# Performance work log

Hardware: AMD Instinct MI355X
Metric: run time of the kernel (lower is better)

## Reference

```python
import jax, jax.numpy as jnp
import numpy as np


def setup_inputs() -> dict:
    key = jax.random.key(0)
    ks = jax.random.split(key, 10)
    B, C, T, H, W = 8, 128, 8, 32, 32
    Cq = C // 8
    return {
        "x": jax.random.normal(ks[0], (B, C, T, H, W), dtype=jnp.float32),
        "Wq": jax.random.normal(ks[1], (Cq, C), dtype=jnp.float32) * (1.0 / np.sqrt(C)),
        "bq": jax.random.normal(ks[2], (Cq,), dtype=jnp.float32) * 0.02,
        "Wk": jax.random.normal(ks[3], (Cq, C), dtype=jnp.float32) * (1.0 / np.sqrt(C)),
        "bk": jax.random.normal(ks[4], (Cq,), dtype=jnp.float32) * 0.02,
        "Wv": jax.random.normal(ks[5], (C, C), dtype=jnp.float32) * (1.0 / np.sqrt(C)),
        "bv": jax.random.normal(ks[6], (C,), dtype=jnp.float32) * 0.02,
        "gamma_pam": jax.random.normal(ks[7], (1,), dtype=jnp.float32),
        "gamma_cam": jax.random.normal(ks[8], (1,), dtype=jnp.float32),
        "gamma_tim": jax.random.normal(ks[9], (1,), dtype=jnp.float32),
    }


def reference(x, Wq, bq, Wk, bk, Wv, bv, gamma_pam, gamma_cam, gamma_tim):
    B, C, T, H, W = x.shape
    HW = H * W

    # ---- PAM: position attention over HW, feature dim = (C//8)*T ----
    # 1x1x1 Conv3d == per-position channel matmul
    q = jnp.einsum('bcthw,oc->bothw', x, Wq) + bq[None, :, None, None, None]
    k = jnp.einsum('bcthw,oc->bothw', x, Wk) + bk[None, :, None, None, None]
    v = jnp.einsum('bcthw,oc->bothw', x, Wv) + bv[None, :, None, None, None]
    qf = q.reshape(B, -1, HW)   # [B, (C//8)*T, HW]
    kf = k.reshape(B, -1, HW)
    vf = v.reshape(B, -1, HW)   # [B, C*T, HW]
    energy = jnp.einsum('bcn,bcm->bnm', qf, kf)          # [B, HW, HW]
    attn = jax.nn.softmax(energy, axis=-1)
    # out = bmm(v, attn^T)
    pam = jnp.einsum('bcm,bnm->bcn', vf, attn).reshape(B, C, T, H, W)
    pam = gamma_pam * pam + x

    # ---- CAM: channel attention (C x C) with negated-energy softmax ----
    xc = x.reshape(B, C, -1)                              # [B, C, T*HW]
    e = jnp.einsum('bcn,bdn->bcd', xc, xc)                # [B, C, C]
    e = jnp.max(e, axis=-1, keepdims=True) - e
    a = jax.nn.softmax(e, axis=-1)
    cam = jnp.einsum('bcd,bdn->bcn', a, xc).reshape(B, C, T, H, W)
    cam = gamma_cam * cam + x

    # ---- TIM: temporal attention (T x T) with negated-energy softmax ----
    xt = jnp.transpose(x, (0, 2, 1, 3, 4)).reshape(B, T, -1)  # [B, T, C*HW]
    e = jnp.einsum('btn,bsn->bts', xt, xt)                # [B, T, T]
    e = jnp.max(e, axis=-1, keepdims=True) - e
    a = jax.nn.softmax(e, axis=-1)
    tim = jnp.einsum('bts,bsn->btn', a, xt).reshape(B, T, C, H, W)
    tim = jnp.transpose(tim, (0, 2, 1, 3, 4))
    tim = gamma_tim * tim + x

    return pam + cam + tim
```

## Files before the change

### kernel.cpp

```cpp
#include <hip/hip_runtime.h>
#include <cstdint>

typedef unsigned short u16;
typedef __attribute__((ext_vector_type(8))) short bf16x8;
typedef __attribute__((ext_vector_type(8))) unsigned short u16x8;
typedef __attribute__((ext_vector_type(4))) float f32x4;

constexpr int B_  = 8;
constexpr int C_  = 128;
constexpr int T_  = 8;
constexpr int HW_ = 1024;
constexpr int P_  = T_ * HW_;
constexpr int F_  = 128;
constexpr int CT_ = C_ * T_;

static __device__ __forceinline__ u16 f2bf(float f) {
    union { float f; unsigned u; } v; v.f = f;
    unsigned r = v.u + 0x7fffu + ((v.u >> 16) & 1u);
    return (u16)(r >> 16);
}
static __device__ __forceinline__ float bf2f(u16 h) {
    union { unsigned u; float f; } v; v.u = ((unsigned)h) << 16;
    return v.f;
}

#define GLOAD16(src, dst)                                                     \
    __builtin_amdgcn_global_load_lds(                                         \
        (const __attribute__((address_space(1))) void*)(src),                 \
        (__attribute__((address_space(3))) void*)(dst), 16, 0, 0)

__global__ __launch_bounds__(256)
void k_tim_gram(const float* __restrict__ x, float* __restrict__ e_t,
                const float* __restrict__ Wq, const float* __restrict__ Wk,
                const float* __restrict__ Wv, u16* __restrict__ Wall)
{
    const int b = blockIdx.y, cc = blockIdx.x;
    const int tid = threadIdx.x;

    if (cc == 0 && b == 0) {
        for (int i = tid; i < 20480; i += 256) {
            int oc = i >> 7, c2 = i & 127;
            float wv;
            if (oc < 16)      wv = Wq[oc * 128 + c2];
            else if (oc < 32) wv = Wk[(oc - 16) * 128 + c2];
            else              wv = Wv[(oc - 32) * 128 + c2];
            Wall[i] = f2bf(wv);
        }
    }

    const int hw = tid * 4;
    float4 xv[2][8];
    #pragma unroll
    for (int ci = 0; ci < 2; ci++) {
        const float* xb = x + ((size_t)(b * C_ + cc * 2 + ci)) * P_;
        #pragma unroll
        for (int t = 0; t < 8; t++)
            xv[ci][t] = *(const float4*)&xb[t * HW_ + hw];
    }

    float acc[36];
    #pragma unroll
    for (int p = 0; p < 36; p++) acc[p] = 0.f;
    #pragma unroll
    for (int ci = 0; ci < 2; ci++) {
        int p = 0;
        #pragma unroll
        for (int t = 0; t < 8; t++)
            #pragma unroll
            for (int s = t; s < 8; s++) {
                float4 a = xv[ci][t], c4 = xv[ci][s];
                acc[p++] += a.x * c4.x + a.y * c4.y + a.z * c4.z + a.w * c4.w;
            }
    }

    const int lane = tid & 63, w = tid >> 6;
    #pragma unroll
    for (int p = 0; p < 36; p++)
        #pragma unroll
        for (int off = 32; off; off >>= 1)
            acc[p] += __shfl_xor(acc[p], off);

    __shared__ float sm[4][36];
    if (lane == 0)
        #pragma unroll
        for (int p = 0; p < 36; p++) sm[w][p] = acc[p];
    __syncthreads();
    if (tid < 36) {
        float v = sm[0][tid] + sm[1][tid] + sm[2][tid] + sm[3][tid];
        int t = 0, rem = tid;
        while (rem >= 8 - t) { rem -= 8 - t; t++; }
        int s = t + rem;
        atomicAdd(&e_t[b * 64 + t * 8 + s], v);
        if (s != t) atomicAdd(&e_t[b * 64 + s * 8 + t], v);
    }
}

__global__ __launch_bounds__(256)
void k_prep(const float* __restrict__ x, u16* __restrict__ xT,
            u16* __restrict__ xhi, u16* __restrict__ xlo,
            const u16* __restrict__ Wall,
            const float* __restrict__ bq, const float* __restrict__ bk,
            const float* __restrict__ bv,
            u16* __restrict__ qt, u16* __restrict__ kt, u16* __restrict__ v16)
{
    __shared__ char sy[32768];
    const int b  = blockIdx.y;
    const int p0 = blockIdx.x * 128;
    const int tid = threadIdx.x, lane = tid & 63, w = tid >> 6;

    #pragma unroll
    for (int r = 0; r < 16; r++) {
        int lin = r * 256 + tid;
        int c = lin >> 5, j4 = (lin & 31) << 2;
        size_t gi = ((size_t)(b * C_ + c)) * P_ + p0 + j4;
        float4 xv = *(const float4*)&x[gi];
        float a4[4] = {xv.x, xv.y, xv.z, xv.w};
        ushort4 h, l;
        h.x = f2bf(a4[0]); h.y = f2bf(a4[1]);
        h.z = f2bf(a4[2]); h.w = f2bf(a4[3]);
        l.x = f2bf(a4[0] - bf2f(h.x)); l.y = f2bf(a4[1] - bf2f(h.y));
        l.z = f2bf(a4[2] - bf2f(h.z)); l.w = f2bf(a4[3] - bf2f(h.w));
        *(ushort4*)&xhi[gi] = h;
        *(ushort4*)&xlo[gi] = l;
        #pragma unroll
        for (int u = 0; u < 4; u++) {
            int pi = j4 + u;
            int byte = pi * 256 + ((c * 2) ^ (((pi >> 2) & 15) << 4));
            *(u16*)(sy + byte) = (u == 0) ? h.x : (u == 1) ? h.y
                               : (u == 2) ? h.z : h.w;
        }
    }
    __syncthreads();

    #pragma unroll
    for (int r = 0; r < 8; r++) {
        int lin = r * 256 + tid;
        int pi = lin >> 4, ci8 = (lin & 15) << 3;
        bf16x8 v = *(const bf16x8*)(sy + pi * 256 +
                                    ((ci8 * 2) ^ (((pi >> 2) & 15) << 4)));
        *(bf16x8*)&xT[((size_t)(b * P_ + p0 + pi)) * C_ + ci8] = v;
    }

    bf16x8 bg[4][2];
    #pragma unroll
    for (int ks = 0; ks < 4; ks++)
        #pragma unroll
        for (int ni = 0; ni < 2; ni++) {
            int p  = w * 32 + ni * 16 + (lane & 15);
            int cb = (ks * 32 + (lane >> 4) * 8) * 2;
            bg[ks][ni] = *(const bf16x8*)(sy + p * 256 +
                              (cb ^ (((p >> 2) & 15) << 4)));
        }
    __syncthreads();

    f32x4 acc[10][2];
    #pragma unroll
    for (int mi = 0; mi < 10; mi++) {
        acc[mi][0] = (f32x4){0.f, 0.f, 0.f, 0.f};
        acc[mi][1] = (f32x4){0.f, 0.f, 0.f, 0.f};
    }

    #pragma unroll
    for (int mi = 0; mi < 10; mi++) {
        #pragma unroll
        for (int ks = 0; ks < 4; ks++) {
            bf16x8 af = *(const bf16x8*)(Wall + (mi * 16 + (lane & 15)) * 128
                                          + ks * 32 + (lane >> 4) * 8);
            acc[mi][0] = __builtin_amdgcn_mfma_f32_16x16x32_bf16(
                af, bg[ks][0], acc[mi][0], 0, 0, 0);
            acc[mi][1] = __builtin_amdgcn_mfma_f32_16x16x32_bf16(
                af, bg[ks][1], acc[mi][1], 0, 0, 0);
        }
    }

    const int t      = p0 >> 10;
    const int hw0    = p0 & 1023;
    const int hwbase = hw0 + w * 32;

    #pragma unroll
    for (int mi = 2; mi < 10; mi++)
        #pragma unroll
        for (int ni = 0; ni < 2; ni++)
            #pragma unroll
            for (int r = 0; r < 4; r++) {
                int oc = mi * 16 + (lane >> 4) * 4 + r;
                int hw = hwbase + ni * 16 + (lane & 15);
                v16[((size_t)(b * C_ + oc - 32)) * P_ + t * HW_ + hw] =
                    f2bf(acc[mi][ni][r] + bv[oc - 32]);
            }

    u16* qk = (u16*)sy;
    #pragma unroll
    for (int mi = 0; mi < 2; mi++)
        #pragma unroll
        for (int ni = 0; ni < 2; ni++) {
            int hwl = w * 32 + ni * 16 + (lane & 15);
            int cq0 = (lane >> 4) * 4;
            ushort4 pk;
            float b0 = (mi == 0) ? bq[cq0 + 0] : bk[cq0 + 0];
            float b1 = (mi == 0) ? bq[cq0 + 1] : bk[cq0 + 1];
            float b2 = (mi == 0) ? bq[cq0 + 2] : bk[cq0 + 2];
            float b3 = (mi == 0) ? bq[cq0 + 3] : bk[cq0 + 3];
            pk.x = f2bf(acc[mi][ni][0] + b0);
            pk.y = f2bf(acc[mi][ni][1] + b1);
            pk.z = f2bf(acc[mi][ni][2] + b2);
            pk.w = f2bf(acc[mi][ni][3] + b3);
            *(ushort4*)&qk[(mi * 128 + hwl) * 24 + cq0] = pk;
        }
    __syncthreads();
    {
        int mi = tid >> 7, hwl = tid & 127;
        u16x8 lo = *(const u16x8*)&qk[(mi * 128 + hwl) * 24 + 0];
        u16x8 hi = *(const u16x8*)&qk[(mi * 128 + hwl) * 24 + 8];
        u16* dst = (mi == 0) ? qt : kt;
        size_t off = ((size_t)b * HW_ + hw0 + hwl) * F_ + t * 16;
        *(u16x8*)&dst[off]     = lo;
        *(u16x8*)&dst[off + 8] = hi;
    }
}

__global__ __launch_bounds__(256)
void k_attn(const u16* __restrict__ qt, const u16* __restrict__ kt,
            u16* __restrict__ A16)
{
    __shared__ u16 ost[16][1032];
    __shared__ float red[4][16];
    const int b  = blockIdx.y;
    const int n0 = blockIdx.x * 16;
    const int tid = threadIdx.x, lane = tid & 63, w = tid >> 6;
    const u16* qb = qt + (size_t)b * HW_ * F_;
    const u16* kb = kt + (size_t)b * HW_ * F_;

    bf16x8 af[4];
    #pragma unroll
    for (int ks = 0; ks < 4; ks++)
        af[ks] = *(const bf16x8*)(qb + (size_t)(n0 + (lane & 15)) * F_
                                  + ks * 32 + (lane >> 4) * 8);

    f32x4 acc[16];
    #pragma unroll
    for (int j = 0; j < 16; j++) acc[j] = (f32x4){0.f, 0.f, 0.f, 0.f};

    #pragma unroll
    for (int j = 0; j < 16; j++) {
        const int m0 = w * 256 + j * 16;
        #pragma unroll
        for (int ks = 0; ks < 4; ks++) {
            bf16x8 bg = *(const bf16x8*)(kb + (size_t)(m0 + (lane & 15)) * F_
                                         + ks * 32 + (lane >> 4) * 8);
            acc[j] = __builtin_amdgcn_mfma_f32_16x16x32_bf16(
                af[ks], bg, acc[j], 0, 0, 0);
        }
    }

    float rmax[4];
    #pragma unroll
    for (int r = 0; r < 4; r++) {
        float m = acc[0][r];
        #pragma unroll
        for (int j = 1; j < 16; j++) m = fmaxf(m, acc[j][r]);
        #pragma unroll
        for (int off = 1; off < 16; off <<= 1) m = fmaxf(m, __shfl_xor(m, off));
        rmax[r] = m;
    }
    if ((lane & 15) == 0)
        #pragma unroll
        for (int r = 0; r < 4; r++) red[w][(lane >> 4) * 4 + r] = rmax[r];
    __syncthreads();
    #pragma unroll
    for (int r = 0; r < 4; r++) {
        int row = (lane >> 4) * 4 + r;
        rmax[r] = fmaxf(fmaxf(red[0][row], red[1][row]),
                        fmaxf(red[2][row], red[3][row]));
    }
    __syncthreads();

    float rsum[4];
    #pragma unroll
    for (int r = 0; r < 4; r++) {
        float s = 0.f;
        #pragma unroll
        for (int j = 0; j < 16; j++) {
            acc[j][r] = __expf(acc[j][r] - rmax[r]);
            s += acc[j][r];
        }
        #pragma unroll
        for (int off = 1; off < 16; off <<= 1) s += __shfl_xor(s, off);
        rsum[r] = s;
    }
    if ((lane & 15) == 0)
        #pragma unroll
        for (int r = 0; r < 4; r++) red[w][(lane >> 4) * 4 + r] = rsum[r];
    __syncthreads();

    #pragma unroll
    for (int r = 0; r < 4; r++) {
        int row = (lane >> 4) * 4 + r;
        float inv = 1.0f / (red[0][row] + red[1][row] +
                            red[2][row] + red[3][row]);
        #pragma unroll
        for (int j = 0; j < 16; j++)
            ost[row][w * 256 + j * 16 + (lane & 15)] = f2bf(acc[j][r] * inv);
    }
    __syncthreads();

    u16* ob = A16 + ((size_t)b * HW_ + n0) * HW_;
    #pragma unroll
    for (int it = 0; it < 8; it++) {
        int lin = it * 256 + tid;
        int row = lin >> 7, g = lin & 127;
        *(u16x8*)&ob[(size_t)row * HW_ + g * 8] = *(const u16x8*)&ost[row][g * 8];
    }
}

__global__ __launch_bounds__(256)
void k_pv(const u16* __restrict__ v16, const u16* __restrict__ A16,
          const float* __restrict__ gamma_pam, u16* __restrict__ pam16)
{
    __shared__ char As[2][16384];
    __shared__ char Bs[2][16384];
    const int b   = blockIdx.z;
    const int ct0 = blockIdx.y * 128, n0 = blockIdx.x * 128;
    const int tid = threadIdx.x, lane = tid & 63, w = tid >> 6;
    const u16* vb = v16 + (size_t)b * CT_ * HW_;
    const u16* ab = A16 + (size_t)b * HW_ * HW_;

    const int s_row = (lane >> 3);
    const int s_col = ((lane & 7) ^ ((lane >> 3) & 7)) * 8;

    const int wr = w >> 1, wc = w & 1;
    f32x4 acc[4][4];
    #pragma unroll
    for (int mi = 0; mi < 4; mi++)
        #pragma unroll
        for (int ni = 0; ni < 4; ni++) acc[mi][ni] = (f32x4){0.f, 0.f, 0.f, 0.f};

    #pragma unroll
    for (int i = 0; i < 4; i++) {
        int c = w * 4 + i;
        int row = c * 8 + s_row;
        GLOAD16(vb + (size_t)(ct0 + row) * HW_ + s_col, As[0] + c * 1024);
        GLOAD16(ab + (size_t)(n0  + row) * HW_ + s_col, Bs[0] + c * 1024);
    }
    __syncthreads();

    int cur = 0;
    for (int it = 0; it < 16; ++it) {
        if (it < 15) {
            int mc = (it + 1) * 64;
            #pragma unroll
            for (int i = 0; i < 4; i++) {
                int c = w * 4 + i;
                int row = c * 8 + s_row;
                GLOAD16(vb + (size_t)(ct0 + row) * HW_ + mc + s_col,
                        As[cur ^ 1] + c * 1024);
                GLOAD16(ab + (size_t)(n0  + row) * HW_ + mc + s_col,
                        Bs[cur ^ 1] + c * 1024);
            }
        }
        const char* Ac = As[cur];
        const char* Bc = Bs[cur];
        #pragma unroll
        for (int ks = 0; ks < 2; ks++) {
            bf16x8 af[4], bg[4];
            #pragma unroll
            for (int mi = 0; mi < 4; mi++) {
                int row  = wr * 64 + mi * 16 + (lane & 15);
                int slot = (ks * 4 + (lane >> 4)) ^ (row & 7);
                af[mi] = *(const bf16x8*)(Ac + row * 128 + slot * 16);
                int rb  = wc * 64 + mi * 16 + (lane & 15);
                int sb  = (ks * 4 + (lane >> 4)) ^ (rb & 7);
                bg[mi] = *(const bf16x8*)(Bc + rb * 128 + sb * 16);
            }
            #pragma unroll
            for (int mi = 0; mi < 4; mi++)
                #pragma unroll
                for (int ni = 0; ni < 4; ni++)
                    acc[mi][ni] = __builtin_amdgcn_mfma_f32_16x16x32_bf16(
                        af[mi], bg[ni], acc[mi][ni], 0, 0, 0);
        }
        __syncthreads();
        cur ^= 1;
    }

    const float gp = gamma_pam[0];
    u16* ot = (u16*)As;
    #pragma unroll
    for (int mi = 0; mi < 4; mi++)
        #pragma unroll
        for (int ni = 0; ni < 4; ni++)
            #pragma unroll
            for (int r = 0; r < 4; r++)
                ot[(wr * 64 + mi * 16 + (lane >> 4) * 4 + r) * 128 +
                   wc * 64 + ni * 16 + (lane & 15)] = f2bf(gp * acc[mi][ni][r]);
    __syncthreads();

    u16* ob = pam16 + (size_t)b * CT_ * HW_;
    #pragma unroll
    for (int it = 0; it < 8; it++) {
        int lin = it * 256 + tid;
        int row = lin >> 4, col = (lin & 15) * 8;
        *(u16x8*)&ob[(size_t)(ct0 + row) * HW_ + n0 + col] =
            *(const u16x8*)&ot[row * 128 + col];
    }
}

__global__ __launch_bounds__(256)
void k_cam_gram(const u16* __restrict__ xhi, const u16* __restrict__ xlo,
                float* __restrict__ part)
{
    __shared__ char Sh[32768];
    __shared__ char Sl[32768];
    const int b = blockIdx.y, ch = blockIdx.x;
    const int tid = threadIdx.x, lane = tid & 63, w = tid >> 6;
    const u16* hb = xhi + (size_t)b * C_ * P_;
    const u16* lb = xlo + (size_t)b * C_ * P_;

    f32x4 acc[8][2];
    #pragma unroll
    for (int mi = 0; mi < 8; mi++) {
        acc[mi][0] = (f32x4){0.f, 0.f, 0.f, 0.f};
        acc[mi][1] = (f32x4){0.f, 0.f, 0.f, 0.f};
    }

    for (int kc = 0; kc < 2; kc++) {
        int n0 = ch * 256 + kc * 128;
        #pragma unroll
        for (int i = 0; i < 8; i++) {
            int c4  = w * 8 + i;
            int row = c4 * 4 + (lane >> 4);
            int col = ((lane & 15) ^ (row & 7)) * 8;
            GLOAD16(hb + (size_t)row * P_ + n0 + col, Sh + c4 * 1024);
            GLOAD16(lb + (size_t)row * P_ + n0 + col, Sl + c4 * 1024);
        }
        __syncthreads();
        #pragma unroll
        for (int ks = 0; ks < 4; ks++) {
            bf16x8 bh[2], bl[2];
            #pragma unroll
            for (int ni = 0; ni < 2; ni++) {
                int rb = w * 32 + ni * 16 + (lane & 15);
                int sb = (ks * 4 + (lane >> 4)) ^ (rb & 7);
                bh[ni] = *(const bf16x8*)(Sh + rb * 256 + sb * 16);
                bl[ni] = *(const bf16x8*)(Sl + rb * 256 + sb * 16);
            }
            #pragma unroll
            for (int mi = 0; mi < 8; mi++) {
                int ra = mi * 16 + (lane & 15);
                int sa = (ks * 4 + (lane >> 4)) ^ (ra & 7);
                bf16x8 ah = *(const bf16x8*)(Sh + ra * 256 + sa * 16);
                bf16x8 al = *(const bf16x8*)(Sl + ra * 256 + sa * 16);
                #pragma unroll
                for (int ni = 0; ni < 2; ni++) {
                    acc[mi][ni] = __builtin_amdgcn_mfma_f32_16x16x32_bf16(
                        ah, bh[ni], acc[mi][ni], 0, 0, 0);
                    acc[mi][ni] = __builtin_amdgcn_mfma_f32_16x16x32_bf16(
                        ah, bl[ni], acc[mi][ni], 0, 0, 0);
                    acc[mi][ni] = __builtin_amdgcn_mfma_f32_16x16x32_bf16(
                        al, bh[ni], acc[mi][ni], 0, 0, 0);
                }
            }
        }
        __syncthreads();
    }

    float* pb = part + ((size_t)(b * 32 + ch)) * 16384;
    #pragma unroll
    for (int mi = 0; mi < 8; mi++)
        #pragma unroll
        for (int ni = 0; ni < 2; ni++)
            #pragma unroll
            for (int r = 0; r < 4; r++) {
                int c = mi * 16 + (lane >> 4) * 4 + r;
                int d = w * 32 + ni * 16 + (lane & 15);
                pb[c * 128 + d] = acc[mi][ni][r];
            }
}

__global__ __launch_bounds__(128)
void k_cam_reduce(const float* __restrict__ part,
                  const float* __restrict__ gamma_cam, u16* __restrict__ acam16)
{
    const int b = blockIdx.y, c = blockIdx.x;
    const int d = threadIdx.x;
    float s = 0.f;
    for (int ch = 0; ch < 32; ch++)
        s += part[(((size_t)(b * 32 + ch)) * C_ + c) * C_ + d];
    float mn = s;
    #pragma unroll
    for (int off = 32; off; off >>= 1) mn = fminf(mn, __shfl_xor(mn, off));
    __shared__ float m1[2], m2[2];
    if ((d & 63) == 0) m1[d >> 6] = mn;
    __syncthreads();
    mn = fminf(m1[0], m1[1]);
    float p = __expf(mn - s);
    float sum = p;
    #pragma unroll
    for (int off = 32; off; off >>= 1) sum += __shfl_xor(sum, off);
    if ((d & 63) == 0) m2[d >> 6] = sum;
    __syncthreads();
    sum = m2[0] + m2[1];
    acam16[((size_t)(b * C_ + c)) * C_ + d] = f2bf(gamma_cam[0] * p / sum);
}

__global__ __launch_bounds__(256)
void k_xprime(const float* __restrict__ x, const float* __restrict__ e_t,
              const float* __restrict__ gamma_tim, u16* __restrict__ Xp)
{
    const int b = blockIdx.y, c = blockIdx.x;
    const size_t base = ((size_t)(b * C_ + c)) * P_;
    const int tid = threadIdx.x;
    const float gt = gamma_tim[0];

    float4 xv[8];
    #pragma unroll
    for (int t = 0; t < 8; t++)
        xv[t] = *(const float4*)&x[base + t * HW_ + tid * 4];

    #pragma unroll
    for (int t = 0; t < 8; t++) {
        float e[8];
        #pragma unroll
        for (int s = 0; s < 8; s++) e[s] = e_t[b * 64 + t * 8 + s];
        float mn = e[0];
        #pragma unroll
        for (int s = 1; s < 8; s++) mn = fminf(mn, e[s]);
        float p[8], sum = 0.f;
        #pragma unroll
        for (int s = 0; s < 8; s++) { p[s] = __expf(mn - e[s]); sum += p[s]; }
        float inv = gt / sum;

        float4 o = make_float4(3.f * xv[t].x, 3.f * xv[t].y,
                               3.f * xv[t].z, 3.f * xv[t].w);
        #pragma unroll
        for (int s = 0; s < 8; s++) {
            float wgt = p[s] * inv;
            o.x += wgt * xv[s].x; o.y += wgt * xv[s].y;
            o.z += wgt * xv[s].z; o.w += wgt * xv[s].w;
        }
        ushort4 pk;
        pk.x = f2bf(o.x); pk.y = f2bf(o.y); pk.z = f2bf(o.z); pk.w = f2bf(o.w);
        *(ushort4*)&Xp[base + t * HW_ + tid * 4] = pk;
    }
}

__global__ __launch_bounds__(256)
void k_cam_av(const u16* __restrict__ acam16, const u16* __restrict__ xT,
              const u16* __restrict__ Xp, const u16* __restrict__ pam16,
              float* __restrict__ out)
{
    const int b  = blockIdx.y;
    const int p0 = blockIdx.x * 128;
    const int tid = threadIdx.x, lane = tid & 63, w = tid >> 6;

    const u16* Ab = acam16 + (size_t)b * C_ * C_;
    const u16* Bb = xT + ((size_t)(b * P_ + p0 + w * 32)) * C_;

    f32x4 acc[8][2];
    #pragma unroll
    for (int mi = 0; mi < 8; mi++) {
        acc[mi][0] = (f32x4){0.f, 0.f, 0.f, 0.f};
        acc[mi][1] = (f32x4){0.f, 0.f, 0.f, 0.f};
    }

    bf16x8 bg[4][2];
    #pragma unroll
    for (int ks = 0; ks < 4; ks++)
        #pragma unroll
        for (int ni = 0; ni < 2; ni++)
            bg[ks][ni] = *(const bf16x8*)(Bb +
                (size_t)(ni * 16 + (lane & 15)) * C_ + ks * 32 + (lane >> 4) * 8);

    #pragma unroll
    for (int mi = 0; mi < 8; mi++) {
        #pragma unroll
        for (int ks = 0; ks < 4; ks++) {
            bf16x8 af = *(const bf16x8*)(Ab +
                (size_t)(mi * 16 + (lane & 15)) * C_ + ks * 32 + (lane >> 4) * 8);
            acc[mi][0] = __builtin_amdgcn_mfma_f32_16x16x32_bf16(
                af, bg[ks][0], acc[mi][0], 0, 0, 0);
            acc[mi][1] = __builtin_amdgcn_mfma_f32_16x16x32_bf16(
                af, bg[ks][1], acc[mi][1], 0, 0, 0);
        }
    }

    const int tt = p0 >> 10;
    float* ob = out + (size_t)b * C_ * P_;
    const u16* xp = Xp + (size_t)b * C_ * P_;
    const u16* pb = pam16 + (size_t)b * CT_ * HW_;
    #pragma unroll
    for (int mi = 0; mi < 8; mi++)
        #pragma unroll
        for (int ni = 0; ni < 2; ni++)
            #pragma unroll
            for (int r = 0; r < 4; r++) {
                int c = mi * 16 + (lane >> 4) * 4 + r;
                int p = p0 + w * 32 + ni * 16 + (lane & 15);
                int hw = p & 1023;
                size_t i = (size_t)c * P_ + p;
                float pam = bf2f(pb[((size_t)(c * 8 + tt)) * HW_ + hw]);
                ob[i] = pam + acc[mi][ni][r] + bf2f(xp[i]);
            }
}

extern "C" void kernel_launch(void* const* d_in, const int* in_sizes, int n_in,
                              void* d_out, int out_size, void* d_ws, size_t ws_size,
                              hipStream_t stream)
{
    (void)in_sizes; (void)n_in; (void)out_size; (void)ws_size;
    const float* x  = (const float*)d_in[0];
    const float* Wq = (const float*)d_in[1];
    const float* bq = (const float*)d_in[2];
    const float* Wk = (const float*)d_in[3];
    const float* bk = (const float*)d_in[4];
    const float* Wv = (const float*)d_in[5];
    const float* bv = (const float*)d_in[6];
    const float* gp = (const float*)d_in[7];
    const float* gc = (const float*)d_in[8];
    const float* gt = (const float*)d_in[9];
    float* out = (float*)d_out;
    char*  ws  = (char*)d_ws;

    const size_t MiB = 1u << 20;
    u16*   xT     = (u16*)(ws + 0);
    u16*   v16    = (u16*)(ws + 16 * MiB);
    u16*   xhi    = (u16*)(ws + 32 * MiB);
    u16*   xlo    = (u16*)(ws + 48 * MiB);
    u16*   A16    = (u16*)(ws + 64 * MiB);
    u16*   pam16  = (u16*)(ws + 80 * MiB);
    float* part   = (float*)(ws + 96 * MiB);
    u16*   Xp16   = (u16*)(ws + 113 * MiB);
    u16*   qtb    = (u16*)(ws + 130 * MiB);
    u16*   ktb    = (u16*)(ws + 132 * MiB);
    u16*   acam16 = (u16*)(ws + 134 * MiB);
    u16*   Wall   = (u16*)(ws + 134 * MiB + 65536);
    float* etim   = (float*)(ws + 134 * MiB + 131072);

    hipMemsetAsync(etim, 0, 512 * sizeof(float), stream);

    k_tim_gram  <<<dim3(64, 8),   256, 0, stream>>>(x, etim,
                                                    Wq, Wk, Wv, Wall);
    k_prep      <<<dim3(64, 8),   256, 0, stream>>>(x, xT, xhi, xlo, Wall,
                                                    bq, bk, bv,
                                                    qtb, ktb, v16);
    k_attn      <<<dim3(64, 8),   256, 0, stream>>>(qtb, ktb, A16);
    k_pv        <<<dim3(8, 8, 8), 256, 0, stream>>>(v16, A16, gp, pam16);
    k_xprime    <<<dim3(128, 8),  256, 0, stream>>>(x, etim, gt, Xp16);
    k_cam_gram  <<<dim3(32, 8),   256, 0, stream>>>(xhi, xlo, part);
    k_cam_reduce<<<dim3(128, 8),  128, 0, stream>>>(part, gc, acam16);
    k_cam_av    <<<dim3(64, 8),   256, 0, stream>>>(acam16, xT, Xp16,
                                                    pam16, out);
}
```

Measured before the change: 268.5 us.

## Fuse temporal mixing into prep, drop hi/lo staging, retile prep by hw

k_prep now tiles 16 hw positions across all 8 time steps. That lets it compute the temporal-attention mixed tensor Xp from shared memory, which removes the separate k_xprime kernel and its re-read of x. The bf16 hi/lo split buffers are gone: k_cam_gram reads fp32 x directly and does the split in registers, trading a 32 MiB write plus reread for a 64 MiB fp32 read. k_tim_gram now uses one channel per block over twice as many blocks, and the q/k/v outputs are staged through shared memory for coalesced stores. The added prep work and the register-array use in the Xp loop may raise register pressure.

```diff
diff --git a/kernel.cpp b/kernel.cpp
--- a/kernel.cpp
+++ b/kernel.cpp
@@ -34,10 +34,10 @@
                 const float* __restrict__ Wq, const float* __restrict__ Wk,
                 const float* __restrict__ Wv, u16* __restrict__ Wall)
 {
-    const int b = blockIdx.y, cc = blockIdx.x;
+    const int b = blockIdx.y, c = blockIdx.x;
     const int tid = threadIdx.x;
 
-    if (cc == 0 && b == 0) {
+    if (c == 0 && b == 0) {
         for (int i = tid; i < 20480; i += 256) {
             int oc = i >> 7, c2 = i & 127;
             float wv;
@@ -48,28 +48,22 @@
         }
     }
 
+    const float* xb = x + ((size_t)(b * C_ + c)) * P_;
     const int hw = tid * 4;
-    float4 xv[2][8];
-    #pragma unroll
-    for (int ci = 0; ci < 2; ci++) {
-        const float* xb = x + ((size_t)(b * C_ + cc * 2 + ci)) * P_;
+    float4 xv[8];
+    #pragma unroll
+    for (int t = 0; t < 8; t++)
+        xv[t] = *(const float4*)&xb[t * HW_ + hw];
+
+    float acc[36];
+    {
+        int p = 0;
         #pragma unroll
         for (int t = 0; t < 8; t++)
-            xv[ci][t] = *(const float4*)&xb[t * HW_ + hw];
-    }
-
-    float acc[36];
-    #pragma unroll
-    for (int p = 0; p < 36; p++) acc[p] = 0.f;
-    #pragma unroll
-    for (int ci = 0; ci < 2; ci++) {
-        int p = 0;
-        #pragma unroll
-        for (int t = 0; t < 8; t++)
             #pragma unroll
             for (int s = t; s < 8; s++) {
-                float4 a = xv[ci][t], c4 = xv[ci][s];
-                acc[p++] += a.x * c4.x + a.y * c4.y + a.z * c4.z + a.w * c4.w;
+                float4 a = xv[t], c4 = xv[s];
+                acc[p++] = a.x * c4.x + a.y * c4.y + a.z * c4.z + a.w * c4.w;
             }
     }
 
@@ -96,39 +90,49 @@
 }
 
 __global__ __launch_bounds__(256)
-void k_prep(const float* __restrict__ x, u16* __restrict__ xT,
-            u16* __restrict__ xhi, u16* __restrict__ xlo,
+void k_prep(const float* __restrict__ x, const float* __restrict__ e_t,
             const u16* __restrict__ Wall,
             const float* __restrict__ bq, const float* __restrict__ bk,
-            const float* __restrict__ bv,
-            u16* __restrict__ qt, u16* __restrict__ kt, u16* __restrict__ v16)
+            const float* __restrict__ bv, const float* __restrict__ gamma_tim,
+            u16* __restrict__ xT, u16* __restrict__ qt, u16* __restrict__ kt,
+            u16* __restrict__ v16, u16* __restrict__ Xp)
 {
     __shared__ char sy[32768];
-    const int b  = blockIdx.y;
-    const int p0 = blockIdx.x * 128;
+    __shared__ u16  qk[4096];
+    __shared__ float wgt[8][8];
+    const int b   = blockIdx.y;
+    const int hw0 = blockIdx.x * 16;
     const int tid = threadIdx.x, lane = tid & 63, w = tid >> 6;
 
     #pragma unroll
     for (int r = 0; r < 16; r++) {
         int lin = r * 256 + tid;
-        int c = lin >> 5, j4 = (lin & 31) << 2;
-        size_t gi = ((size_t)(b * C_ + c)) * P_ + p0 + j4;
-        float4 xv = *(const float4*)&x[gi];
+        int c = lin >> 5;
+        int rem = lin & 31;
+        int t = rem >> 2, j4 = (rem & 3) << 2;
+        float4 xv = *(const float4*)&x[((size_t)(b * C_ + c)) * P_
+                                       + t * HW_ + hw0 + j4];
         float a4[4] = {xv.x, xv.y, xv.z, xv.w};
-        ushort4 h, l;
-        h.x = f2bf(a4[0]); h.y = f2bf(a4[1]);
-        h.z = f2bf(a4[2]); h.w = f2bf(a4[3]);
-        l.x = f2bf(a4[0] - bf2f(h.x)); l.y = f2bf(a4[1] - bf2f(h.y));
-        l.z = f2bf(a4[2] - bf2f(h.z)); l.w = f2bf(a4[3] - bf2f(h.w));
-        *(ushort4*)&xhi[gi] = h;
-        *(ushort4*)&xlo[gi] = l;
         #pragma unroll
         for (int u = 0; u < 4; u++) {
-            int pi = j4 + u;
-            int byte = pi * 256 + ((c * 2) ^ (((pi >> 2) & 15) << 4));
-            *(u16*)(sy + byte) = (u == 0) ? h.x : (u == 1) ? h.y
-                               : (u == 2) ? h.z : h.w;
-        }
+            int pidx = t * 16 + j4 + u;
+            int byte = pidx * 256 + ((c * 2) ^ (((pidx >> 2) & 15) << 4));
+            *(u16*)(sy + byte) = f2bf(a4[u]);
+        }
+    }
+    if (tid < 8) {
+        float e[8];
+        #pragma unroll
+        for (int s = 0; s < 8; s++) e[s] = e_t[b * 64 + tid * 8 + s];
+        float mn = e[0];
+        #pragma unroll
+        for (int s = 1; s < 8; s++) mn = fminf(mn, e[s]);
+        float p[8], sum = 0.f;
+        #pragma unroll
+        for (int s = 0; s < 8; s++) { p[s] = __expf(mn - e[s]); sum += p[s]; }
+        float inv = gamma_tim[0] / sum;
+        #pragma unroll
+        for (int s = 0; s < 8; s++) wgt[tid][s] = p[s] * inv;
     }
     __syncthreads();
 
@@ -138,7 +142,33 @@
         int pi = lin >> 4, ci8 = (lin & 15) << 3;
         bf16x8 v = *(const bf16x8*)(sy + pi * 256 +
                                     ((ci8 * 2) ^ (((pi >> 2) & 15) << 4)));
-        *(bf16x8*)&xT[((size_t)(b * P_ + p0 + pi)) * C_ + ci8] = v;
+        int pg = (pi >> 4) * HW_ + hw0 + (pi & 15);
+        *(bf16x8*)&xT[((size_t)(b * P_ + pg)) * C_ + ci8] = v;
+    }
+
+    {
+        int c = tid >> 1, g = tid & 1;
+        float xsv[8][8];
+        #pragma unroll
+        for (int t = 0; t < 8; t++)
+            #pragma unroll
+            for (int k = 0; k < 8; k++) {
+                int pidx = t * 16 + g * 8 + k;
+                int byte = pidx * 256 + ((c * 2) ^ (((pidx >> 2) & 15) << 4));
+                xsv[t][k] = bf2f(*(const u16*)(sy + byte));
+            }
+        #pragma unroll
+        for (int t = 0; t < 8; t++) {
+            u16x8 pk;
+            #pragma unroll
+            for (int k = 0; k < 8; k++) {
+                float o = 3.f * xsv[t][k];
+                #pragma unroll
+                for (int s = 0; s < 8; s++) o += wgt[t][s] * xsv[s][k];
+                pk[k] = f2bf(o);
+            }
+            *(u16x8*)&Xp[((size_t)(b * C_ + c)) * P_ + t * HW_ + hw0 + g * 8] = pk;
+        }
     }
 
     bf16x8 bg[4][2];
@@ -159,7 +189,6 @@
         acc[mi][0] = (f32x4){0.f, 0.f, 0.f, 0.f};
         acc[mi][1] = (f32x4){0.f, 0.f, 0.f, 0.f};
     }
-
     #pragma unroll
     for (int mi = 0; mi < 10; mi++) {
         #pragma unroll
@@ -173,49 +202,47 @@
         }
     }
 
-    const int t      = p0 >> 10;
-    const int hw0    = p0 & 1023;
-    const int hwbase = hw0 + w * 32;
-
-    #pragma unroll
-    for (int mi = 2; mi < 10; mi++)
+    u16* vt = (u16*)sy;
+    #pragma unroll
+    for (int mi = 0; mi < 10; mi++)
         #pragma unroll
         for (int ni = 0; ni < 2; ni++)
             #pragma unroll
             for (int r = 0; r < 4; r++) {
-                int oc = mi * 16 + (lane >> 4) * 4 + r;
-                int hw = hwbase + ni * 16 + (lane & 15);
-                v16[((size_t)(b * C_ + oc - 32)) * P_ + t * HW_ + hw] =
-                    f2bf(acc[mi][ni][r] + bv[oc - 32]);
-            }
-
-    u16* qk = (u16*)sy;
-    #pragma unroll
-    for (int mi = 0; mi < 2; mi++)
-        #pragma unroll
-        for (int ni = 0; ni < 2; ni++) {
-            int hwl = w * 32 + ni * 16 + (lane & 15);
-            int cq0 = (lane >> 4) * 4;
-            ushort4 pk;
-            float b0 = (mi == 0) ? bq[cq0 + 0] : bk[cq0 + 0];
-            float b1 = (mi == 0) ? bq[cq0 + 1] : bk[cq0 + 1];
-            float b2 = (mi == 0) ? bq[cq0 + 2] : bk[cq0 + 2];
-            float b3 = (mi == 0) ? bq[cq0 + 3] : bk[cq0 + 3];
-            pk.x = f2bf(acc[mi][ni][0] + b0);
-            pk.y = f2bf(acc[mi][ni][1] + b1);
-            pk.z = f2bf(acc[mi][ni][2] + b2);
-            pk.w = f2bf(acc[mi][ni][3] + b3);
-            *(ushort4*)&qk[(mi * 128 + hwl) * 24 + cq0] = pk;
-        }
-    __syncthreads();
-    {
-        int mi = tid >> 7, hwl = tid & 127;
-        u16x8 lo = *(const u16x8*)&qk[(mi * 128 + hwl) * 24 + 0];
-        u16x8 hi = *(const u16x8*)&qk[(mi * 128 + hwl) * 24 + 8];
-        u16* dst = (mi == 0) ? qt : kt;
-        size_t off = ((size_t)b * HW_ + hw0 + hwl) * F_ + t * 16;
-        *(u16x8*)&dst[off]     = lo;
-        *(u16x8*)&dst[off + 8] = hi;
+                int oc   = mi * 16 + (lane >> 4) * 4 + r;
+                int pidx = w * 32 + ni * 16 + (lane & 15);
+                float bias;
+                if (mi == 0)      bias = bq[oc];
+                else if (mi == 1) bias = bk[oc - 16];
+                else              bias = bv[oc - 32];
+                u16 val = f2bf(acc[mi][ni][r] + bias);
+                if (oc < 32) {
+                    int m = oc >> 4, cq = oc & 15;
+                    qk[m * 2048 + (pidx & 15) * 128 + (pidx >> 4) * 16 + cq] = val;
+                } else {
+                    int c = oc - 32;
+                    int byte = c * 256 + ((pidx * 2) ^ ((c & 7) << 4));
+                    *(u16*)((char*)vt + byte) = val;
+                }
+            }
+    __syncthreads();
+
+    #pragma unroll
+    for (int it = 0; it < 8; it++) {
+        int lin = it * 256 + tid;
+        int c = lin >> 4, tg = lin & 15;
+        int t = tg >> 1, g = tg & 1;
+        int pb2 = (t * 16 + g * 8) * 2;
+        u16x8 vv = *(const u16x8*)(sy + c * 256 + (pb2 ^ ((c & 7) << 4)));
+        *(u16x8*)&v16[((size_t)(b * C_ + c)) * P_ + t * HW_ + hw0 + g * 8] = vv;
+    }
+    #pragma unroll
+    for (int it = 0; it < 2; it++) {
+        int lin = it * 256 + tid;
+        int m = lin >> 8, hwl = (lin >> 4) & 15, ck = lin & 15;
+        u16x8 vv = *(const u16x8*)&qk[m * 2048 + hwl * 128 + ck * 8];
+        u16* dst = m ? kt : qt;
+        *(u16x8*)&dst[((size_t)b * HW_ + hw0 + hwl) * F_ + ck * 8] = vv;
     }
 }
 
@@ -406,15 +433,13 @@
 }
 
 __global__ __launch_bounds__(256)
-void k_cam_gram(const u16* __restrict__ xhi, const u16* __restrict__ xlo,
-                float* __restrict__ part)
+void k_cam_gram(const float* __restrict__ x, float* __restrict__ part)
 {
     __shared__ char Sh[32768];
     __shared__ char Sl[32768];
     const int b = blockIdx.y, ch = blockIdx.x;
     const int tid = threadIdx.x, lane = tid & 63, w = tid >> 6;
-    const u16* hb = xhi + (size_t)b * C_ * P_;
-    const u16* lb = xlo + (size_t)b * C_ * P_;
+    const float* xb = x + (size_t)b * C_ * P_;
 
     f32x4 acc[8][2];
     #pragma unroll
@@ -426,12 +451,20 @@
     for (int kc = 0; kc < 2; kc++) {
         int n0 = ch * 256 + kc * 128;
         #pragma unroll
-        for (int i = 0; i < 8; i++) {
-            int c4  = w * 8 + i;
-            int row = c4 * 4 + (lane >> 4);
-            int col = ((lane & 15) ^ (row & 7)) * 8;
-            GLOAD16(hb + (size_t)row * P_ + n0 + col, Sh + c4 * 1024);
-            GLOAD16(lb + (size_t)row * P_ + n0 + col, Sl + c4 * 1024);
+        for (int r = 0; r < 16; r++) {
+            int lin = r * 256 + tid;
+            int c = lin >> 5, j4 = (lin & 31) << 2;
+            float4 xv = *(const float4*)&xb[(size_t)c * P_ + n0 + j4];
+            float a4[4] = {xv.x, xv.y, xv.z, xv.w};
+            ushort4 h, l;
+            h.x = f2bf(a4[0]); h.y = f2bf(a4[1]);
+            h.z = f2bf(a4[2]); h.w = f2bf(a4[3]);
+            l.x = f2bf(a4[0] - bf2f(h.x)); l.y = f2bf(a4[1] - bf2f(h.y));
+            l.z = f2bf(a4[2] - bf2f(h.z)); l.w = f2bf(a4[3] - bf2f(h.w));
+            int grp = j4 >> 3, off = (j4 & 7) * 2;
+            int byteb = c * 256 + ((grp ^ (c & 7)) << 4) + off;
+            *(ushort4*)(Sh + byteb) = h;
+            *(ushort4*)(Sl + byteb) = l;
         }
         __syncthreads();
         #pragma unroll
@@ -504,47 +537,6 @@
 }
 
 __global__ __launch_bounds__(256)
-void k_xprime(const float* __restrict__ x, const float* __restrict__ e_t,
-              const float* __restrict__ gamma_tim, u16* __restrict__ Xp)
-{
-    const int b = blockIdx.y, c = blockIdx.x;
-    const size_t base = ((size_t)(b * C_ + c)) * P_;
-    const int tid = threadIdx.x;
-    const float gt = gamma_tim[0];
-
-    float4 xv[8];
-    #pragma unroll
-    for (int t = 0; t < 8; t++)
-        xv[t] = *(const float4*)&x[base + t * HW_ + tid * 4];
-
-    #pragma unroll
-    for (int t = 0; t < 8; t++) {
-        float e[8];
-        #pragma unroll
-        for (int s = 0; s < 8; s++) e[s] = e_t[b * 64 + t * 8 + s];
-        float mn = e[0];
-        #pragma unroll
-        for (int s = 1; s < 8; s++) mn = fminf(mn, e[s]);
-        float p[8], sum = 0.f;
-        #pragma unroll
-        for (int s = 0; s < 8; s++) { p[s] = __expf(mn - e[s]); sum += p[s]; }
-        float inv = gt / sum;
-
-        float4 o = make_float4(3.f * xv[t].x, 3.f * xv[t].y,
-                               3.f * xv[t].z, 3.f * xv[t].w);
-        #pragma unroll
-        for (int s = 0; s < 8; s++) {
-            float wgt = p[s] * inv;
-            o.x += wgt * xv[s].x; o.y += wgt * xv[s].y;
-            o.z += wgt * xv[s].z; o.w += wgt * xv[s].w;
-        }
-        ushort4 pk;
-        pk.x = f2bf(o.x); pk.y = f2bf(o.y); pk.z = f2bf(o.z); pk.w = f2bf(o.w);
-        *(ushort4*)&Xp[base + t * HW_ + tid * 4] = pk;
-    }
-}
-
-__global__ __launch_bounds__(256)
 void k_cam_av(const u16* __restrict__ acam16, const u16* __restrict__ xT,
               const u16* __restrict__ Xp, const u16* __restrict__ pam16,
               float* __restrict__ out)
@@ -624,29 +616,26 @@
     const size_t MiB = 1u << 20;
     u16*   xT     = (u16*)(ws + 0);
     u16*   v16    = (u16*)(ws + 16 * MiB);
-    u16*   xhi    = (u16*)(ws + 32 * MiB);
-    u16*   xlo    = (u16*)(ws + 48 * MiB);
-    u16*   A16    = (u16*)(ws + 64 * MiB);
-    u16*   pam16  = (u16*)(ws + 80 * MiB);
-    float* part   = (float*)(ws + 96 * MiB);
-    u16*   Xp16   = (u16*)(ws + 113 * MiB);
-    u16*   qtb    = (u16*)(ws + 130 * MiB);
-    u16*   ktb    = (u16*)(ws + 132 * MiB);
-    u16*   acam16 = (u16*)(ws + 134 * MiB);
-    u16*   Wall   = (u16*)(ws + 134 * MiB + 65536);
-    float* etim   = (float*)(ws + 134 * MiB + 131072);
+    u16*   A16    = (u16*)(ws + 32 * MiB);
+    u16*   pam16  = (u16*)(ws + 48 * MiB);
+    float* part   = (float*)(ws + 64 * MiB);
+    u16*   Xp16   = (u16*)(ws + 80 * MiB);
+    u16*   qtb    = (u16*)(ws + 96 * MiB);
+    u16*   ktb    = (u16*)(ws + 98 * MiB);
+    u16*   acam16 = (u16*)(ws + 100 * MiB);
+    u16*   Wall   = (u16*)(ws + 100 * MiB + 65536);
+    float* etim   = (float*)(ws + 100 * MiB + 131072);
 
     hipMemsetAsync(etim, 0, 512 * sizeof(float), stream);
 
-    k_tim_gram  <<<dim3(64, 8),   256, 0, stream>>>(x, etim,
+    k_tim_gram  <<<dim3(128, 8),  256, 0, stream>>>(x, etim,
                                                     Wq, Wk, Wv, Wall);
-    k_prep      <<<dim3(64, 8),   256, 0, stream>>>(x, xT, xhi, xlo, Wall,
-                                                    bq, bk, bv,
-                                                    qtb, ktb, v16);
+    k_prep      <<<dim3(64, 8),   256, 0, stream>>>(x, etim, Wall,
+                                                    bq, bk, bv, gt,
+                                                    xT, qtb, ktb, v16, Xp16);
     k_attn      <<<dim3(64, 8),   256, 0, stream>>>(qtb, ktb, A16);
     k_pv        <<<dim3(8, 8, 8), 256, 0, stream>>>(v16, A16, gp, pam16);
-    k_xprime    <<<dim3(128, 8),  256, 0, stream>>>(x, etim, gt, Xp16);
-    k_cam_gram  <<<dim3(32, 8),   256, 0, stream>>>(xhi, xlo, part);
+    k_cam_gram  <<<dim3(32, 8),   256, 0, stream>>>(x, part);
     k_cam_reduce<<<dim3(128, 8),  128, 0, stream>>>(part, gc, acam16);
     k_cam_av    <<<dim3(64, 8),   256, 0, stream>>>(acam16, xT, Xp16,
                                                     pam16, out);
```

Result: faster. 261.5 us (-2.6%).
